# Kernel optimization log

Hardware: AMD Instinct MI355X
Metric: run time of the kernel (lower is better)

The kernel has to match this reference:

```python
import jax, jax.numpy as jnp
import numpy as np

E = 1024
FF = 4096
EPS = 1e-5


def _linear(x, W, b):
    # x: [B,S,in], W: [in,out], b: [out]
    return jnp.einsum('bsi,io->bso', x, W) + b


def _layernorm(x, g, b):
    mu = jnp.mean(x, axis=-1, keepdims=True)
    var = jnp.mean(jnp.square(x - mu), axis=-1, keepdims=True)
    return (x - mu) * jax.lax.rsqrt(var + EPS) * g + b


def setup_inputs() -> dict:
    key = jax.random.key(0)
    ks = jax.random.split(key, 8)
    s = 0.02
    inp = {
        'src': jax.random.normal(ks[0], (4, 2048, E), dtype=jnp.float32),
        'Wq': jax.random.normal(ks[1], (E, E), dtype=jnp.float32) * s,
        'bq': jnp.zeros((E,), jnp.float32),
        'Wk': jax.random.normal(ks[2], (E, E), dtype=jnp.float32) * s,
        'bk': jnp.zeros((E,), jnp.float32),
        'Wv': jax.random.normal(ks[3], (E, E), dtype=jnp.float32) * s,
        'bv': jnp.zeros((E,), jnp.float32),
        'Wo': jax.random.normal(ks[4], (E, E), dtype=jnp.float32) * s,
        'bo': jnp.zeros((E,), jnp.float32),
        'W1': jax.random.normal(ks[5], (E, FF), dtype=jnp.float32) * s,
        'b1': jnp.zeros((FF,), jnp.float32),
        'W2': jax.random.normal(ks[6], (FF, E), dtype=jnp.float32) * s,
        'b2': jnp.zeros((E,), jnp.float32),
        'g1': jnp.ones((E,), jnp.float32),
        'be1': jnp.zeros((E,), jnp.float32),
        'g2': jnp.ones((E,), jnp.float32),
        'be2': jnp.zeros((E,), jnp.float32),
    }
    return inp


def reference(src, Wq, bq, Wk, bk, Wv, bv, Wo, bo, W1, b1, W2, b2, g1, be1, g2, be2):
    Q = _linear(src, Wq, bq)
    K = _linear(src, Wk, bk)
    V = _linear(src, Wv, bv)
    # Single-head attention, NO 1/sqrt(d) scaling (faithful to source)
    scores = jnp.einsum('bqe,bke->bqk', Q, K)  # [B,S,S]
    weights = jax.nn.softmax(scores, axis=-1)
    attn = jnp.einsum('bqk,bke->bqe', weights, V)
    attn = _linear(attn, Wo, bo)
    x = _layernorm(src + attn, g1, be1)
    ff = _linear(x, W1, b1)
    ff = jax.nn.relu(ff)
    ff = _linear(ff, W2, b2)
    return _layernorm(x + ff, g2, be2)
```

## Files before the change

### kernel.cpp

```cpp
#include <hip/hip_runtime.h>
#include <hip/hip_bf16.h>


using u16 = unsigned short;
typedef __attribute__((ext_vector_type(8))) _Float16 half8;
typedef __attribute__((ext_vector_type(4))) float f32x4;

#define BATCH 4
#define SEQ   2048
#define EMB   1024
#define FFD   4096

#define SWZ(r) ((((r) >> 1) & 3) << 4)

__device__ __forceinline__ u16 f2h(float f) {
    union { _Float16 h; u16 u; } x;
    x.h = (_Float16)f;
    return x.u;
}
__device__ __forceinline__ float h2f(u16 u) {
    union { u16 u; _Float16 h; } x;
    x.u = u;
    return (float)x.h;
}

typedef const __attribute__((address_space(1))) void* gas_ptr;
typedef __attribute__((address_space(3))) void* las_ptr;

__device__ __forceinline__ void load_lds16(const void* g, void* l) {
    __builtin_amdgcn_global_load_lds((gas_ptr)g, (las_ptr)l, 16, 0, 0);
}

template <typename OutT, bool RELU, bool BIAS>
__global__ __launch_bounds__(512, 2) void gemm_8p(
    const u16* __restrict__ A, const u16* __restrict__ Bt,
    OutT* __restrict__ C, const float* __restrict__ bias,
    int N, int K, int lda, int ldb, int ldc, long sA, long sB, long sC)
{
    constexpr int BUF = 65536;
    __shared__ __attribute__((aligned(16))) char lds[2 * BUF];

    A  += (long)blockIdx.z * sA;
    Bt += (long)blockIdx.z * sB;
    C  += (long)blockIdx.z * sC;

    const int tid  = threadIdx.x;
    const int lane = tid & 63;
    const int wv   = tid >> 6;
    const int wm   = wv >> 2;
    const int wn   = wv & 3;
    const long row0 = (long)blockIdx.x * 256;
    const long col0 = (long)blockIdx.y * 256;

    long aS[2], bS[2]; int dD[2];
#pragma unroll
    for (int i = 0; i < 2; ++i) {
        const int d16 = i * 512 + tid;
        const int lrow = d16 >> 3;
        const int sl   = d16 & 7;
        const long cswz = (long)((sl ^ (lrow & 7)) << 3);
        aS[i] = (row0 + lrow) * (long)lda + cswz;
        bS[i] = (col0 + lrow) * (long)ldb + cswz;
        dD[i] = d16 * 16;
    }
    const long aHop = 128 * (long)lda;
    const long bHop = 128 * (long)ldb;

    const int klb = (lane >> 4) << 4;
    const int swz = (lane & 7) << 4;
    const int aRB = (wm * 128 + (lane & 15)) * 128 + (klb ^ swz);
    const int bRB = 32768 + (wn * 64 + (lane & 15)) * 128 + (klb ^ swz);

    f32x4 acc[8][4] = {};
    half8 a[8], b[4];
    const int G = K >> 6;

#define SGA(BUFB, H, KT)                                                      \
    { _Pragma("unroll") for (int i_ = 0; i_ < 2; ++i_)                        \
          load_lds16(A + aS[i_] + (H) * aHop + (long)(KT) * 64,               \
                     lds + (BUFB) + (H) * 16384 + dD[i_]); }
#define SGB(BUFB, H, KT)                                                      \
    { _Pragma("unroll") for (int i_ = 0; i_ < 2; ++i_)                        \
          load_lds16(Bt + bS[i_] + (H) * bHop + (long)(KT) * 64,              \
                     lds + (BUFB) + 32768 + (H) * 16384 + dD[i_]); }
#define NOP8 ((void)0)
#define VM8 asm volatile("s_waitcnt vmcnt(8)" ::: "memory")
#define VM6 asm volatile("s_waitcnt vmcnt(6)" ::: "memory")
#define VM2 asm volatile("s_waitcnt vmcnt(2)" ::: "memory")
#define VMZ asm volatile("s_waitcnt vmcnt(0)" ::: "memory")

#define PH8(BUFB, QM, QN, RDA, RDB, STG, VM)                                  \
    {                                                                         \
        if (RDA) {                                                            \
            _Pragma("unroll") for (int m_ = 0; m_ < 4; ++m_)                  \
            _Pragma("unroll") for (int k_ = 0; k_ < 2; ++k_)                  \
                a[m_ * 2 + k_] = *(const half8*)(lds + (BUFB) +               \
                    ((aRB + (QM) * 8192 + m_ * 2048) ^ (k_ << 6)));           \
        }                                                                     \
        if (RDB) {                                                            \
            _Pragma("unroll") for (int n_ = 0; n_ < 2; ++n_)                  \
            _Pragma("unroll") for (int k_ = 0; k_ < 2; ++k_)                  \
                b[n_ * 2 + k_] = *(const half8*)(lds + (BUFB) +               \
                    ((bRB + (QN) * 4096 + n_ * 2048) ^ (k_ << 6)));           \
        }                                                                     \
        STG; VM;                                                              \
        __builtin_amdgcn_s_barrier();                                         \
        __builtin_amdgcn_s_setprio(1);                                        \
        _Pragma("unroll") for (int k_ = 0; k_ < 2; ++k_)                      \
        _Pragma("unroll") for (int m_ = 0; m_ < 4; ++m_)                      \
        _Pragma("unroll") for (int n_ = 0; n_ < 2; ++n_)                      \
            acc[(QM) * 4 + m_][(QN) * 2 + n_] =                               \
                __builtin_amdgcn_mfma_f32_16x16x32_f16(                       \
                    a[m_ * 2 + k_], b[n_ * 2 + k_],                           \
                    acc[(QM) * 4 + m_][(QN) * 2 + n_], 0, 0, 0);              \
        __builtin_amdgcn_s_setprio(0);                                        \
        __builtin_amdgcn_s_barrier();                                         \
    }

    SGA(0, 0, 0); SGB(0, 1, 0); SGB(0, 0, 0); SGA(0, 1, 0);
    SGA(BUF, 0, 1); SGB(BUF, 1, 1);
    VM6;
    __builtin_amdgcn_s_barrier();

    for (int t = 0; t < G - 2; ++t) {
        const int cb = (t & 1) * BUF, ob = cb ^ BUF;
        PH8(cb, 0, 0, 1, 1, SGB(ob, 0, t + 1), NOP8)
        PH8(cb, 0, 1, 0, 1, SGA(ob, 1, t + 1), VM8)
        PH8(cb, 1, 1, 1, 0, SGA(cb, 0, t + 2), NOP8)
        PH8(cb, 1, 0, 0, 1, SGB(cb, 1, t + 2), VM6)
    }
    {
        const int cb = ((G - 2) & 1) * BUF, ob = cb ^ BUF;
        PH8(cb, 0, 0, 1, 1, SGB(ob, 0, G - 1), NOP8)
        PH8(cb, 0, 1, 0, 1, SGA(ob, 1, G - 1), VM8)
        PH8(cb, 1, 1, 1, 0, NOP8, NOP8)
        PH8(cb, 1, 0, 0, 1, NOP8, VM2)
    }
    {
        const int cb = ((G - 1) & 1) * BUF;
        PH8(cb, 0, 0, 1, 1, NOP8, NOP8)
        PH8(cb, 0, 1, 0, 1, NOP8, VMZ)
        PH8(cb, 1, 1, 1, 0, NOP8, NOP8)
        PH8(cb, 1, 0, 0, 1, NOP8, NOP8)
    }
#undef PH8
#undef SGA
#undef SGB
#undef NOP8
#undef VM8
#undef VM6
#undef VM2
#undef VMZ

    long cofs[4]; float bb[4];
#pragma unroll
    for (int n = 0; n < 4; ++n) {
        cofs[n] = col0 + wn * 64 + (n >> 1) * 32 + (n & 1) * 16 + (lane & 15);
        bb[n] = BIAS ? bias[cofs[n]] : 0.0f;
    }
#pragma unroll
    for (int m = 0; m < 8; ++m) {
#pragma unroll
        for (int r = 0; r < 4; ++r) {
            const long row = row0 + wm * 128 + (m >> 2) * 64 + (m & 3) * 16 +
                             ((lane >> 4) << 2) + r;
            OutT* Crow = C + row * (long)ldc;
#pragma unroll
            for (int n = 0; n < 4; ++n) {
                float v = acc[m][n][r] + bb[n];
                if (RELU) v = fmaxf(v, 0.0f);
                if constexpr (sizeof(OutT) == 2)
                    Crow[cofs[n]] = f2h(v);
                else
                    Crow[cofs[n]] = v;
            }
        }
    }
}

template <int BM, typename OutT, bool RELU, int BMODE>
__global__ __launch_bounds__(512, 2) void gemm_dp(
    const u16* __restrict__ A, const u16* __restrict__ Bt,
    OutT* __restrict__ C, const float* __restrict__ bias,
    int N, int K, int lda, int ldb, int ldc, long sA, long sB, long sC)
{
    constexpr int MF = BM / 32;
    constexpr int AL = BM / 128;
    constexpr int SLAB_A = BM * 32;
    constexpr int SLAB_B = 256 * 32;

    __shared__ u16 ldsA[4 * SLAB_A];
    __shared__ u16 ldsB[4 * SLAB_B];

    A  += (long)blockIdx.z * sA;
    Bt += (long)blockIdx.z * sB;
    C  += (long)blockIdx.z * sC;

    const int tid  = threadIdx.x;
    const int lane = tid & 63;
    const int wv   = tid >> 6;
    const int wm   = wv >> 2;
    const int wn   = wv & 3;
    const long row0 = (long)blockIdx.x * BM;
    const long col0 = (long)blockIdx.y * 256;

    long aoff[AL]; int adst[AL];
#pragma unroll
    for (int i = 0; i < AL; ++i) {
        const int d16 = i * 512 + tid;
        const int row = d16 >> 2;
        const int colb = ((d16 & 3) << 4) ^ SWZ(row);
        aoff[i] = (row0 + row) * (long)lda + (colb >> 1);
        adst[i] = d16 * 16;
    }
    long boff[2]; int bdst[2];
#pragma unroll
    for (int i = 0; i < 2; ++i) {
        const int d16 = i * 512 + tid;
        const int row = d16 >> 2;
        const int colb = ((d16 & 3) << 4) ^ SWZ(row);
        boff[i] = (col0 + row) * (long)ldb + (colb >> 1);
        bdst[i] = d16 * 16;
    }

    int aro[MF], bro[4];
    const int klane = (lane >> 4) << 4;
#pragma unroll
    for (int m = 0; m < MF; ++m) {
        const int row = wm * (BM / 2) + m * 16 + (lane & 15);
        aro[m] = row * 64 + (klane ^ SWZ(row));
    }
#pragma unroll
    for (int n = 0; n < 4; ++n) {
        const int row = wn * 64 + n * 16 + (lane & 15);
        bro[n] = row * 64 + (klane ^ SWZ(row));
    }

    f32x4 acc[MF][4] = {};
    const int G = K >> 5;

    auto stage = [&](int g) {
        const int slot = g & 3;
        const long k0 = (long)g << 5;
#pragma unroll
        for (int i = 0; i < AL; ++i)
            load_lds16(A + aoff[i] + k0, (char*)ldsA + slot * (SLAB_A * 2) + adst[i]);
#pragma unroll
        for (int i = 0; i < 2; ++i)
            load_lds16(Bt + boff[i] + k0, (char*)ldsB + slot * (SLAB_B * 2) + bdst[i]);
    };

#define VMS asm volatile("s_waitcnt vmcnt(6)" ::: "memory")
#define VMT asm volatile("s_waitcnt vmcnt(3)" ::: "memory")
#define VM0 asm volatile("s_waitcnt vmcnt(0)" ::: "memory")
#define VMNONE ((void)0)

#define GBODY(g, VMASM, DOSTAGE)                                              \
    {                                                                         \
        const int slot_ = (g) & 3;                                            \
        const char* abase_ = (const char*)ldsA + slot_ * (SLAB_A * 2);        \
        const char* bbase_ = (const char*)ldsB + slot_ * (SLAB_B * 2);        \
        half8 a_[MF], b_[4];                                                  \
        _Pragma("unroll") for (int m = 0; m < MF; ++m)                        \
            a_[m] = *(const half8*)(abase_ + aro[m]);                         \
        _Pragma("unroll") for (int n = 0; n < 4; ++n)                         \
            b_[n] = *(const half8*)(bbase_ + bro[n]);                         \
        if (DOSTAGE) stage((g) + 3);                                          \
        VMASM;                                                                \
        __builtin_amdgcn_s_setprio(1);                                        \
        _Pragma("unroll") for (int m = 0; m < MF; ++m)                        \
            _Pragma("unroll") for (int n = 0; n < 4; ++n)                     \
                acc[m][n] = __builtin_amdgcn_mfma_f32_16x16x32_f16(           \
                    a_[m], b_[n], acc[m][n], 0, 0, 0);                        \
        __builtin_amdgcn_s_setprio(0);                                        \
        __builtin_amdgcn_s_barrier();                                         \
    }

    stage(0); stage(1); stage(2);
    VMS;
    __builtin_amdgcn_s_barrier();

    for (int g = 0; g < G - 3; ++g) GBODY(g, VMS, true)
    GBODY(G - 3, VMT, false)
    GBODY(G - 2, VM0, false)
    GBODY(G - 1, VMNONE, false)
#undef GBODY
#undef VMS
#undef VMT
#undef VM0
#undef VMNONE

#pragma unroll
    for (int n = 0; n < 4; ++n) {
        const long col = col0 + wn * 64 + n * 16 + (lane & 15);
        const float bc_ = (BMODE == 1) ? bias[col] : 0.0f;
#pragma unroll
        for (int m = 0; m < MF; ++m) {
            const long row = row0 + wm * (BM / 2) + m * 16 + ((lane >> 4) << 2);
#pragma unroll
            for (int r = 0; r < 4; ++r) {
                float v = acc[m][n][r] + bc_;
                if (BMODE == 2) v += bias[row + r];
                if (RELU) v = fmaxf(v, 0.0f);
                if constexpr (sizeof(OutT) == 2)
                    C[(row + r) * (long)ldc + col] = f2h(v);
                else
                    C[(row + r) * (long)ldc + col] = v;
            }
        }
    }
}

__global__ __launch_bounds__(256) void tc4(
    const float* __restrict__ s0, const float* __restrict__ s1,
    const float* __restrict__ s2, const float* __restrict__ s3,
    u16* __restrict__ dqk, u16* __restrict__ dwv, u16* __restrict__ dwo)
{
    __shared__ float t[32][33];
    const int z = blockIdx.z;
    const float* in = (z == 0) ? s0 : (z == 1) ? s1 : (z == 2) ? s2 : s3;
    u16* out = (z < 2) ? (dqk + (long)z * EMB * EMB) : (z == 2 ? dwv : dwo);
    const int bc = blockIdx.x * 32, br = blockIdx.y * 32;
    const int lx = threadIdx.x & 31, ly = threadIdx.x >> 5;
#pragma unroll
    for (int i = 0; i < 32; i += 8)
        t[ly + i][lx] = in[(long)(br + ly + i) * EMB + bc + lx];
    __syncthreads();
#pragma unroll
    for (int i = 0; i < 32; i += 8)
        out[(long)(bc + ly + i) * EMB + br + lx] = f2h(t[lx][ly + i]);
}

__global__ __launch_bounds__(256) void transpose_cast(
    const float* __restrict__ in, u16* __restrict__ out, int R, int C)
{
    __shared__ float t[32][33];
    const int bc = blockIdx.x * 32, br = blockIdx.y * 32;
    const int lx = threadIdx.x & 31, ly = threadIdx.x >> 5;
#pragma unroll
    for (int i = 0; i < 32; i += 8)
        t[ly + i][lx] = in[(long)(br + ly + i) * C + bc + lx];
    __syncthreads();
#pragma unroll
    for (int i = 0; i < 32; i += 8)
        out[(long)(bc + ly + i) * R + br + lx] = f2h(t[lx][ly + i]);
}

__global__ __launch_bounds__(256) void cast_h(
    const float* __restrict__ in, u16* __restrict__ out)
{
    const long i = ((long)blockIdx.x * 256 + threadIdx.x) * 8;
    const float4 a = ((const float4*)(in + i))[0];
    const float4 b = ((const float4*)(in + i))[1];
    union { u16 u[8]; uint4 v; } pk;
    pk.u[0] = f2h(a.x); pk.u[1] = f2h(a.y); pk.u[2] = f2h(a.z); pk.u[3] = f2h(a.w);
    pk.u[4] = f2h(b.x); pk.u[5] = f2h(b.y); pk.u[6] = f2h(b.z); pk.u[7] = f2h(b.w);
    *(uint4*)(out + i) = pk.v;
}

__global__ __launch_bounds__(256) void concat_bias(
    const float* __restrict__ bq, const float* __restrict__ bk,
    float* __restrict__ o)
{
    const int i = blockIdx.x * 256 + threadIdx.x;
    o[i] = i < 1024 ? bq[i] : bk[i - 1024];
}

__global__ __launch_bounds__(256) void softmax_kernel(
    const u16* __restrict__ S, u16* __restrict__ P)
{
    const long row = blockIdx.x;
    const int tid = threadIdx.x;

    union { uint4 v; u16 u[8]; } in;
    in.v = ((const uint4*)(S + row * SEQ))[tid];
    float f[8];
#pragma unroll
    for (int j = 0; j < 8; ++j) f[j] = h2f(in.u[j]);

    float m = fmaxf(fmaxf(fmaxf(f[0], f[1]), fmaxf(f[2], f[3])),
                    fmaxf(fmaxf(f[4], f[5]), fmaxf(f[6], f[7])));
#pragma unroll
    for (int off = 32; off; off >>= 1) m = fmaxf(m, __shfl_xor(m, off));

    __shared__ float rm[4], rs[4];
    if ((tid & 63) == 0) rm[tid >> 6] = m;
    __syncthreads();
    m = fmaxf(fmaxf(rm[0], rm[1]), fmaxf(rm[2], rm[3]));

    float e[8], s = 0.0f;
#pragma unroll
    for (int j = 0; j < 8; ++j) { e[j] = expf(f[j] - m); s += e[j]; }
#pragma unroll
    for (int off = 32; off; off >>= 1) s += __shfl_xor(s, off);
    if ((tid & 63) == 0) rs[tid >> 6] = s;
    __syncthreads();
    s = (rs[0] + rs[1]) + (rs[2] + rs[3]);

    const float inv = 1.0f / s;
    union { u16 u[8]; uint4 v; } pk;
#pragma unroll
    for (int j = 0; j < 8; ++j) pk.u[j] = f2h(e[j] * inv);
    *(uint4*)(P + row * SEQ + tid * 8) = pk.v;
}

template <bool A16, bool OUT16>
__global__ __launch_bounds__(256) void ln_kernel(
    const void* __restrict__ Ain, const u16* __restrict__ Bin,
    const float* __restrict__ g, const float* __restrict__ be,
    void* __restrict__ Out)
{
    const long row = blockIdx.x;
    const int tid = threadIdx.x;

    float a0, a1, a2, a3;
    if constexpr (A16) {
        union { uint2 v; u16 u[4]; } av;
        av.v = ((const uint2*)((const u16*)Ain + row * EMB))[tid];
        a0 = h2f(av.u[0]); a1 = h2f(av.u[1]); a2 = h2f(av.u[2]); a3 = h2f(av.u[3]);
    } else {
        const float4 av = ((const float4*)((const float*)Ain + row * EMB))[tid];
        a0 = av.x; a1 = av.y; a2 = av.z; a3 = av.w;
    }
    union { uint2 v; u16 u[4]; } bv16;
    bv16.v = ((const uint2*)(Bin + row * EMB))[tid];
    const float h0 = a0 + h2f(bv16.u[0]);
    const float h1 = a1 + h2f(bv16.u[1]);
    const float h2 = a2 + h2f(bv16.u[2]);
    const float h3 = a3 + h2f(bv16.u[3]);

    float s = (h0 + h1) + (h2 + h3);
    float q = (h0 * h0 + h1 * h1) + (h2 * h2 + h3 * h3);
#pragma unroll
    for (int off = 32; off; off >>= 1) {
        s += __shfl_xor(s, off);
        q += __shfl_xor(q, off);
    }
    __shared__ float rsm[4], rqm[4];
    if ((tid & 63) == 0) { rsm[tid >> 6] = s; rqm[tid >> 6] = q; }
    __syncthreads();
    s = (rsm[0] + rsm[1]) + (rsm[2] + rsm[3]);
    q = (rqm[0] + rqm[1]) + (rqm[2] + rqm[3]);

    const float mu  = s * (1.0f / EMB);
    const float var = q * (1.0f / EMB) - mu * mu;
    const float rstd = rsqrtf(var + 1e-5f);

    const float4 gv = ((const float4*)g)[tid];
    const float4 bv = ((const float4*)be)[tid];
    const float y0 = (h0 - mu) * rstd * gv.x + bv.x;
    const float y1 = (h1 - mu) * rstd * gv.y + bv.y;
    const float y2 = (h2 - mu) * rstd * gv.z + bv.z;
    const float y3 = (h3 - mu) * rstd * gv.w + bv.w;

    if constexpr (OUT16) {
        union { u16 u[4]; uint2 v; } pk;
        pk.u[0] = f2h(y0); pk.u[1] = f2h(y1);
        pk.u[2] = f2h(y2); pk.u[3] = f2h(y3);
        ((uint2*)((u16*)Out + row * EMB))[tid] = pk.v;
    } else {
        ((float4*)((float*)Out + row * EMB))[tid] = make_float4(y0, y1, y2, y3);
    }
}

extern "C" void kernel_launch(void* const* d_in, const int* in_sizes, int n_in,
                              void* d_out, int out_size, void* d_ws, size_t ws_size,
                              hipStream_t stream)
{
    const float* src = (const float*)d_in[0];
    const float* Wq  = (const float*)d_in[1];
    const float* bq  = (const float*)d_in[2];
    const float* Wk  = (const float*)d_in[3];
    const float* bk  = (const float*)d_in[4];
    const float* Wv  = (const float*)d_in[5];
    const float* bv  = (const float*)d_in[6];
    const float* Wo  = (const float*)d_in[7];
    const float* bo  = (const float*)d_in[8];
    const float* W1  = (const float*)d_in[9];
    const float* b1  = (const float*)d_in[10];
    const float* W2  = (const float*)d_in[11];
    const float* b2  = (const float*)d_in[12];
    const float* g1  = (const float*)d_in[13];
    const float* be1 = (const float*)d_in[14];
    const float* g2  = (const float*)d_in[15];
    const float* be2 = (const float*)d_in[16];
    float* out = (float*)d_out;

    char* ws = (char*)d_ws;
    const size_t MB = 1ull << 20;
    u16*   WqkT    = (u16*)  (ws + 0 * MB);
    u16*   WvT     = (u16*)  (ws + 4 * MB);
    u16*   WoT     = (u16*)  (ws + 6 * MB);
    u16*   W1T     = (u16*)  (ws + 8 * MB);
    u16*   W2T     = (u16*)  (ws + 16 * MB);
    float* bqk     = (float*)(ws + 24 * MB);
    u16*   Xh      = (u16*)  (ws + 25 * MB);
    u16*   QKh     = (u16*)  (ws + 41 * MB);
    u16*   Vt      = (u16*)  (ws + 73 * MB);
    u16*   scoresh = (u16*)  (ws + 89 * MB);
    u16*   P       = (u16*)  (ws + 121 * MB);
    u16*   attn    = (u16*)  (ws + 89 * MB);
    u16*   attnp   = (u16*)  (ws + 105 * MB);
    u16*   x       = (u16*)  (ws + 121 * MB);
    u16*   ff1     = (u16*)  (ws + 41 * MB);
    u16*   ff2     = (u16*)  (ws + 105 * MB);

    const int M = BATCH * SEQ;
    const long SS = (long)SEQ * SEQ;

    tc4<<<dim3(32, 32, 4), 256, 0, stream>>>(Wq, Wk, Wv, Wo, WqkT, WvT, WoT);
    transpose_cast<<<dim3(128, 32, 1), 256, 0, stream>>>(W1, W1T, EMB, FFD);
    transpose_cast<<<dim3(32, 128, 1), 256, 0, stream>>>(W2, W2T, FFD, EMB);
    concat_bias<<<dim3(8), 256, 0, stream>>>(bq, bk, bqk);

    cast_h<<<dim3((M * EMB) / (256 * 8)), 256, 0, stream>>>(src, Xh);

    gemm_8p<u16, false, true><<<dim3(32, 8, 1), 512, 0, stream>>>(
        Xh, WqkT, QKh, bqk, 2048, 1024, 1024, 1024, 2048, 0, 0, 0);

    gemm_dp<128, u16, false, 2><<<dim3(8, 8, BATCH), 512, 0, stream>>>(
        WvT, Xh, Vt, bv, SEQ, 1024, 1024, 1024, SEQ,
        0, (long)SEQ * EMB, (long)EMB * SEQ);

    gemm_8p<u16, false, false><<<dim3(8, 8, BATCH), 512, 0, stream>>>(
        QKh, QKh + 1024, scoresh, nullptr, SEQ, 1024, 2048, 2048, SEQ,
        (long)SEQ * 2048, (long)SEQ * 2048, SS);

    softmax_kernel<<<dim3(M), 256, 0, stream>>>(scoresh, P);

    gemm_dp<128, u16, false, 0><<<dim3(16, 4, BATCH), 512, 0, stream>>>(
        P, Vt, attn, nullptr, EMB, SEQ, SEQ, SEQ, EMB,
        SS, (long)EMB * SEQ, (long)SEQ * EMB);

    gemm_dp<128, u16, false, 1><<<dim3(64, 4, 1), 512, 0, stream>>>(
        attn, WoT, attnp, bo, EMB, EMB, EMB, EMB, EMB, 0, 0, 0);

    ln_kernel<true, true><<<dim3(M), 256, 0, stream>>>(
        Xh, attnp, g1, be1, x);

    gemm_8p<u16, true, true><<<dim3(32, 16, 1), 512, 0, stream>>>(
        x, W1T, ff1, b1, FFD, EMB, EMB, EMB, FFD, 0, 0, 0);

    gemm_dp<128, u16, false, 1><<<dim3(64, 4, 1), 512, 0, stream>>>(
        ff1, W2T, ff2, b2, EMB, FFD, FFD, FFD, EMB, 0, 0, 0);

    ln_kernel<true, false><<<dim3(M), 256, 0, stream>>>(
        x, ff2, g2, be2, out);
}
```

Baseline: 386.3 us.

## Quantize softmax probabilities and V to fp8 and add fp8 PV GEMM

Softmax now writes P as fp8 and the V projection GEMM stores V transposed as fp8. A new gemm_pv8 kernel uses fp8 MFMA with a 4-slot LDS pipeline to compute attention from P and V. This halves the bytes read in the largest attention GEMM and doubles MFMA throughput per instruction. It risks accuracy loss, since probabilities and V values are quantized to 8-bit floats without scaling.

```diff
diff --git a/kernel.cpp b/kernel.cpp
--- a/kernel.cpp
+++ b/kernel.cpp
@@ -3,6 +3,7 @@
 
 
 using u16 = unsigned short;
+using u8  = unsigned char;
 typedef __attribute__((ext_vector_type(8))) _Float16 half8;
 typedef __attribute__((ext_vector_type(4))) float f32x4;
 
@@ -302,11 +303,134 @@
                 float v = acc[m][n][r] + bc_;
                 if (BMODE == 2) v += bias[row + r];
                 if (RELU) v = fmaxf(v, 0.0f);
-                if constexpr (sizeof(OutT) == 2)
+                if constexpr (sizeof(OutT) == 1) {
+                    const int t = __builtin_amdgcn_cvt_pk_fp8_f32(v, 0.0f, 0, false);
+                    C[(row + r) * (long)ldc + col] = (OutT)(t & 0xff);
+                } else if constexpr (sizeof(OutT) == 2) {
                     C[(row + r) * (long)ldc + col] = f2h(v);
-                else
+                } else {
                     C[(row + r) * (long)ldc + col] = v;
+                }
             }
+        }
+    }
+}
+
+__global__ __launch_bounds__(512, 2) void gemm_pv8(
+    const u8* __restrict__ A, const u8* __restrict__ Bt,
+    u16* __restrict__ C,
+    int N, int K, int lda, int ldb, int ldc, long sA, long sB, long sC)
+{
+    constexpr int MF = 4;
+    constexpr int SLAB_A = 128 * 64;
+    constexpr int SLAB_B = 256 * 64;
+
+    __shared__ __attribute__((aligned(16))) u8 ldsA[4 * SLAB_A];
+    __shared__ __attribute__((aligned(16))) u8 ldsB[4 * SLAB_B];
+
+    A  += (long)blockIdx.z * sA;
+    Bt += (long)blockIdx.z * sB;
+    C  += (long)blockIdx.z * sC;
+
+    const int tid  = threadIdx.x;
+    const int lane = tid & 63;
+    const int wv   = tid >> 6;
+    const int wm   = wv >> 2;
+    const int wn   = wv & 3;
+    const long row0 = (long)blockIdx.x * 128;
+    const long col0 = (long)blockIdx.y * 256;
+
+    long aoff; int adst;
+    {
+        const int d = tid, row = d >> 2, s = d & 3;
+        aoff = (row0 + row) * (long)lda + (long)((s ^ (row & 3)) << 4);
+        adst = d * 16;
+    }
+    long boff[2]; int bdst[2];
+#pragma unroll
+    for (int i = 0; i < 2; ++i) {
+        const int d = i * 512 + tid, row = d >> 2, s = d & 3;
+        boff[i] = (col0 + row) * (long)ldb + (long)((s ^ (row & 3)) << 4);
+        bdst[i] = d * 16;
+    }
+
+    int aro[MF], bro[4];
+    const int klg = (lane >> 4) << 3;
+#pragma unroll
+    for (int m = 0; m < MF; ++m) {
+        const int row = wm * 64 + m * 16 + (lane & 15);
+        aro[m] = row * 64 + (klg ^ ((row & 3) << 4));
+    }
+#pragma unroll
+    for (int n = 0; n < 4; ++n) {
+        const int row = wn * 64 + n * 16 + (lane & 15);
+        bro[n] = row * 64 + (klg ^ ((row & 3) << 4));
+    }
+
+    f32x4 acc[MF][4] = {};
+    const int G = K >> 6;
+
+    auto stage = [&](int g) {
+        const int slot = g & 3;
+        const long k0 = (long)g << 6;
+        load_lds16(A + aoff + k0, ldsA + slot * SLAB_A + adst);
+#pragma unroll
+        for (int i = 0; i < 2; ++i)
+            load_lds16(Bt + boff[i] + k0, ldsB + slot * SLAB_B + bdst[i]);
+    };
+
+#define VMS asm volatile("s_waitcnt vmcnt(6)" ::: "memory")
+#define VMT asm volatile("s_waitcnt vmcnt(3)" ::: "memory")
+#define VM0 asm volatile("s_waitcnt vmcnt(0)" ::: "memory")
+#define VMNONE ((void)0)
+
+#define GB8(g, VMASM, DOSTAGE)                                                \
+    {                                                                         \
+        const int slot_ = (g) & 3;                                            \
+        const u8* abase_ = ldsA + slot_ * SLAB_A;                             \
+        const u8* bbase_ = ldsB + slot_ * SLAB_B;                             \
+        long a_[MF][2], b_[4][2];                                             \
+        _Pragma("unroll") for (int m = 0; m < MF; ++m)                        \
+        _Pragma("unroll") for (int k_ = 0; k_ < 2; ++k_)                      \
+            a_[m][k_] = *(const long*)(abase_ + (aro[m] ^ (k_ << 5)));        \
+        _Pragma("unroll") for (int n = 0; n < 4; ++n)                         \
+        _Pragma("unroll") for (int k_ = 0; k_ < 2; ++k_)                      \
+            b_[n][k_] = *(const long*)(bbase_ + (bro[n] ^ (k_ << 5)));        \
+        if (DOSTAGE) stage((g) + 3);                                          \
+        VMASM;                                                                \
+        __builtin_amdgcn_s_setprio(1);                                        \
+        _Pragma("unroll") for (int k_ = 0; k_ < 2; ++k_)                      \
+        _Pragma("unroll") for (int m = 0; m < MF; ++m)                        \
+        _Pragma("unroll") for (int n = 0; n < 4; ++n)                         \
+            acc[m][n] = __builtin_amdgcn_mfma_f32_16x16x32_fp8_fp8(           \
+                a_[m][k_], b_[n][k_], acc[m][n], 0, 0, 0);                    \
+        __builtin_amdgcn_s_setprio(0);                                        \
+        __builtin_amdgcn_s_barrier();                                         \
+    }
+
+    stage(0); stage(1); stage(2);
+    VMS;
+    __builtin_amdgcn_s_barrier();
+
+    for (int g = 0; g < G - 3; ++g) GB8(g, VMS, true)
+    GB8(G - 3, VMT, false)
+    GB8(G - 2, VM0, false)
+    GB8(G - 1, VMNONE, false)
+#undef GB8
+#undef VMS
+#undef VMT
+#undef VM0
+#undef VMNONE
+
+#pragma unroll
+    for (int n = 0; n < 4; ++n) {
+        const long col = col0 + wn * 64 + n * 16 + (lane & 15);
+#pragma unroll
+        for (int m = 0; m < MF; ++m) {
+            const long row = row0 + wm * 64 + m * 16 + ((lane >> 4) << 2);
+#pragma unroll
+            for (int r = 0; r < 4; ++r)
+                C[(row + r) * (long)ldc + col] = f2h(acc[m][n][r]);
         }
     }
 }
@@ -367,7 +491,7 @@
 }
 
 __global__ __launch_bounds__(256) void softmax_kernel(
-    const u16* __restrict__ S, u16* __restrict__ P)
+    const u16* __restrict__ S, u8* __restrict__ P)
 {
     const long row = blockIdx.x;
     const int tid = threadIdx.x;
@@ -398,10 +522,13 @@
     s = (rs[0] + rs[1]) + (rs[2] + rs[3]);
 
     const float inv = 1.0f / s;
-    union { u16 u[8]; uint4 v; } pk;
-#pragma unroll
-    for (int j = 0; j < 8; ++j) pk.u[j] = f2h(e[j] * inv);
-    *(uint4*)(P + row * SEQ + tid * 8) = pk.v;
+    int lo = 0, hi = 0;
+    lo = __builtin_amdgcn_cvt_pk_fp8_f32(e[0] * inv, e[1] * inv, lo, false);
+    lo = __builtin_amdgcn_cvt_pk_fp8_f32(e[2] * inv, e[3] * inv, lo, true);
+    hi = __builtin_amdgcn_cvt_pk_fp8_f32(e[4] * inv, e[5] * inv, hi, false);
+    hi = __builtin_amdgcn_cvt_pk_fp8_f32(e[6] * inv, e[7] * inv, hi, true);
+    uint2 pk2; pk2.x = (unsigned)lo; pk2.y = (unsigned)hi;
+    *(uint2*)(P + row * SEQ + tid * 8) = pk2;
 }
 
 template <bool A16, bool OUT16>
@@ -496,17 +623,17 @@
     float* bqk     = (float*)(ws + 24 * MB);
     u16*   Xh      = (u16*)  (ws + 25 * MB);
     u16*   QKh     = (u16*)  (ws + 41 * MB);
-    u16*   Vt      = (u16*)  (ws + 73 * MB);
-    u16*   scoresh = (u16*)  (ws + 89 * MB);
-    u16*   P       = (u16*)  (ws + 121 * MB);
-    u16*   attn    = (u16*)  (ws + 89 * MB);
-    u16*   attnp   = (u16*)  (ws + 105 * MB);
-    u16*   x       = (u16*)  (ws + 121 * MB);
+    u8*    Vt8     = (u8*)   (ws + 73 * MB);
+    u16*   scoresh = (u16*)  (ws + 81 * MB);
+    u8*    P8      = (u8*)   (ws + 113 * MB);
+    u16*   attn    = (u16*)  (ws + 81 * MB);
+    u16*   attnp   = (u16*)  (ws + 97 * MB);
+    u16*   x       = (u16*)  (ws + 113 * MB);
     u16*   ff1     = (u16*)  (ws + 41 * MB);
-    u16*   ff2     = (u16*)  (ws + 105 * MB);
+    u16*   ff2     = (u16*)  (ws + 129 * MB);
 
     const int M = BATCH * SEQ;
-    const long SS = (long)SEQ * SEQ;
+    const long SSb = (long)SEQ * SEQ;
 
     tc4<<<dim3(32, 32, 4), 256, 0, stream>>>(Wq, Wk, Wv, Wo, WqkT, WvT, WoT);
     transpose_cast<<<dim3(128, 32, 1), 256, 0, stream>>>(W1, W1T, EMB, FFD);
@@ -518,19 +645,19 @@
     gemm_8p<u16, false, true><<<dim3(32, 8, 1), 512, 0, stream>>>(
         Xh, WqkT, QKh, bqk, 2048, 1024, 1024, 1024, 2048, 0, 0, 0);
 
-    gemm_dp<128, u16, false, 2><<<dim3(8, 8, BATCH), 512, 0, stream>>>(
-        WvT, Xh, Vt, bv, SEQ, 1024, 1024, 1024, SEQ,
+    gemm_dp<128, u8, false, 2><<<dim3(8, 8, BATCH), 512, 0, stream>>>(
+        WvT, Xh, Vt8, bv, SEQ, 1024, 1024, 1024, SEQ,
         0, (long)SEQ * EMB, (long)EMB * SEQ);
 
     gemm_8p<u16, false, false><<<dim3(8, 8, BATCH), 512, 0, stream>>>(
         QKh, QKh + 1024, scoresh, nullptr, SEQ, 1024, 2048, 2048, SEQ,
-        (long)SEQ * 2048, (long)SEQ * 2048, SS);
-
-    softmax_kernel<<<dim3(M), 256, 0, stream>>>(scoresh, P);
-
-    gemm_dp<128, u16, false, 0><<<dim3(16, 4, BATCH), 512, 0, stream>>>(
-        P, Vt, attn, nullptr, EMB, SEQ, SEQ, SEQ, EMB,
-        SS, (long)EMB * SEQ, (long)SEQ * EMB);
+        (long)SEQ * 2048, (long)SEQ * 2048, SSb);
+
+    softmax_kernel<<<dim3(M), 256, 0, stream>>>(scoresh, P8);
+
+    gemm_pv8<<<dim3(16, 4, BATCH), 512, 0, stream>>>(
+        P8, Vt8, attn, EMB, SEQ, SEQ, SEQ, EMB,
+        SSb, (long)EMB * SEQ, (long)SEQ * EMB);
 
     gemm_dp<128, u16, false, 1><<<dim3(64, 4, 1), 512, 0, stream>>>(
         attn, WoT, attnp, bo, EMB, EMB, EMB, EMB, EMB, 0, 0, 0);
```

New measurement: 384.3 us. No clear change (-0.5%).
